# Performance work log

Measured on AMD Instinct MI355X. Metric: run time of the kernel, lower is better.

Reference implementation:

```python
import jax, jax.numpy as jnp
import numpy as np

B, T, HID, NH = 8, 4096, 768, 12
HD = HID // NH          # 64
WIN = 128 // 2          # half window = 64 (local_attention=128)
BLK = 64                # block size == half window
THETA = 10000.0         # local_rope_theta
ATTN_SCALING = 1.0      # default rope type


def setup_inputs() -> dict:
    key = jax.random.key(0)
    k1, k2, k3 = jax.random.split(key, 3)
    hidden_states = jax.random.normal(k1, (B, T, HID), jnp.float32)
    attention_mask = jnp.ones((B, T), jnp.bool_)
    Wqkv = jax.random.normal(k2, (3 * HID, HID), jnp.float32) * 0.02
    Wo = jax.random.normal(k3, (HID, HID), jnp.float32) * 0.02
    return {"hidden_states": hidden_states, "attention_mask": attention_mask,
            "Wqkv": Wqkv, "Wo": Wo}


def _rope(x):
    # x: [B, T, NH, HD]; interleaved-pair complex rotation (pairs = reshape(HD//2, 2))
    pos = jnp.arange(T, dtype=jnp.float32)
    inv_freq = 1.0 / (THETA ** (jnp.arange(0, HD, 2, dtype=jnp.float32) / HD))  # [HD/2]
    ang = pos[:, None] * inv_freq[None, :]                 # [T, HD/2]
    cos = jnp.cos(ang)[None, :, None, :]
    sin = jnp.sin(ang)[None, :, None, :]
    pairs = x.reshape(x.shape[:-1] + (HD // 2, 2))
    a, b = pairs[..., 0], pairs[..., 1]
    ra = a * cos - b * sin
    rb = a * sin + b * cos
    return (jnp.stack([ra, rb], axis=-1).reshape(x.shape)) * ATTN_SCALING


def reference(hidden_states, attention_mask, Wqkv, Wo):
    # fused QKV projection (no bias: attention_bias=False)
    qkv = hidden_states @ Wqkv.T                            # [B, T, 3*HID]
    qkv = qkv.reshape(B, T, 3, NH, HD)
    q, k, v = qkv[:, :, 0], qkv[:, :, 1], qkv[:, :, 2]      # [B, T, NH, HD]
    q = _rope(q)
    k = _rope(k)

    # Blocked sliding-window attention: block = 64, each query block attends
    # key blocks {i-1, i, i+1}; exact +/-64 band enforced by mask.
    nb = T // BLK
    pad = [(0, 0), (BLK, BLK), (0, 0), (0, 0)]
    kp = jnp.pad(k, pad)
    vp = jnp.pad(v, pad)
    kb = kp.reshape(B, nb + 2, BLK, NH, HD)
    vb = vp.reshape(B, nb + 2, BLK, NH, HD)
    knb = jnp.concatenate([kb[:, :-2], kb[:, 1:-1], kb[:, 2:]], axis=2)  # [B, nb, 3*BLK, NH, HD]
    vnb = jnp.concatenate([vb[:, :-2], vb[:, 1:-1], vb[:, 2:]], axis=2)
    qb = q.reshape(B, nb, BLK, NH, HD)

    scores = jnp.einsum('bnqhd,bnkhd->bhnqk', qb, knb) / jnp.sqrt(jnp.float32(HD))
    band = jnp.abs(BLK + jnp.arange(BLK)[:, None] - jnp.arange(3 * BLK)[None, :]) <= WIN  # [BLK, 3*BLK]
    mp = jnp.pad(attention_mask.astype(jnp.bool_), [(0, 0), (BLK, BLK)])
    mb = mp.reshape(B, nb + 2, BLK)
    mnb = jnp.concatenate([mb[:, :-2], mb[:, 1:-1], mb[:, 2:]], axis=2)  # [B, nb, 3*BLK]
    mask = band[None, None, None] & mnb[:, None, :, None, :]
    scores = jnp.where(mask, scores, -jnp.inf)
    probs = jax.nn.softmax(scores, axis=-1)
    out = jnp.einsum('bhnqk,bnkhd->bnqhd', probs, vnb)      # [B, nb, BLK, NH, HD]
    out = out.reshape(B, T, HID)
    return out @ Wo.T
```

## Files before the change

kernel.cpp:

```cpp
#include <hip/hip_runtime.h>
#include <hip/hip_bf16.h>

#define T_SEQ 4096
#define NH 12

typedef __bf16 bf16x8 __attribute__((ext_vector_type(8)));
typedef float f32x4 __attribute__((ext_vector_type(4)));
typedef unsigned int uint32;

__device__ __forceinline__ void gload_lds16(const void* g, void* lds) {
    __builtin_amdgcn_global_load_lds((const __attribute__((address_space(1))) void*)g,
                                     (__attribute__((address_space(3))) void*)lds,
                                     16, 0, 0);
}

__device__ __forceinline__ f32x4 mfma16(bf16x8 a, bf16x8 b, f32x4 c) {
    return __builtin_amdgcn_mfma_f32_16x16x32_bf16(a, b, c, 0, 0, 0);
}

__device__ __forceinline__ void store_out(__hip_bfloat16* p, float v) { *p = __float2bfloat16(v); }
__device__ __forceinline__ void store_out(float* p, float v) { *p = v; }

__global__ __launch_bounds__(256) void f32_to_bf16_kernel(const float* __restrict__ src,
                                                          __hip_bfloat16* __restrict__ dst,
                                                          long n8) {
    long i = (long)blockIdx.x * 256 + threadIdx.x;
    if (i >= n8) return;
    float4 a = *(const float4*)(src + i * 8);
    float4 b = *(const float4*)(src + i * 8 + 4);
    __hip_bfloat16 o[8];
    o[0] = __float2bfloat16(a.x); o[1] = __float2bfloat16(a.y);
    o[2] = __float2bfloat16(a.z); o[3] = __float2bfloat16(a.w);
    o[4] = __float2bfloat16(b.x); o[5] = __float2bfloat16(b.y);
    o[6] = __float2bfloat16(b.z); o[7] = __float2bfloat16(b.w);
    *(uint4*)(dst + i * 8) = *(uint4*)o;
}

__global__ __launch_bounds__(256) void prep_kernel(const float* __restrict__ Wqkv,
                                                   const float* __restrict__ Wo,
                                                   __hip_bfloat16* __restrict__ wqkv_bf,
                                                   __hip_bfloat16* __restrict__ wo_bf,
                                                   float2* __restrict__ tab) {
    long i = (long)blockIdx.x * 256 + threadIdx.x;
    if (i < 221184) {
        const float* s = Wqkv + i * 8;
        __hip_bfloat16* d = wqkv_bf + i * 8;
        float4 a = *(const float4*)s, b = *(const float4*)(s + 4);
        __hip_bfloat16 o[8];
        o[0]=__float2bfloat16(a.x); o[1]=__float2bfloat16(a.y);
        o[2]=__float2bfloat16(a.z); o[3]=__float2bfloat16(a.w);
        o[4]=__float2bfloat16(b.x); o[5]=__float2bfloat16(b.y);
        o[6]=__float2bfloat16(b.z); o[7]=__float2bfloat16(b.w);
        *(uint4*)d = *(uint4*)o;
    } else if (i < 294912) {
        long j = i - 221184;
        const float* s = Wo + j * 8;
        __hip_bfloat16* d = wo_bf + j * 8;
        float4 a = *(const float4*)s, b = *(const float4*)(s + 4);
        __hip_bfloat16 o[8];
        o[0]=__float2bfloat16(a.x); o[1]=__float2bfloat16(a.y);
        o[2]=__float2bfloat16(a.z); o[3]=__float2bfloat16(a.w);
        o[4]=__float2bfloat16(b.x); o[5]=__float2bfloat16(b.y);
        o[6]=__float2bfloat16(b.z); o[7]=__float2bfloat16(b.w);
        *(uint4*)d = *(uint4*)o;
    } else if (i < 425984) {
        long j = i - 294912;
        int tpos = (int)(j >> 5), k = (int)(j & 31);
        float invf = powf(10000.0f, -(2.0f * k) / 64.0f);
        float ang = (float)tpos * invf;
        tab[j] = make_float2((float)cos((double)ang), (float)sin((double)ang));
    }
}

template <typename OutT, int K>
__global__ __launch_bounds__(256) void gemm_nt(const __hip_bfloat16* __restrict__ A,
                                               const __hip_bfloat16* __restrict__ Bw,
                                               OutT* __restrict__ C,
                                               int M, int N, int nbn) {
    __shared__ __align__(16) __hip_bfloat16 As[128 * 64];
    __shared__ __align__(16) __hip_bfloat16 Bs[128 * 64];
    const int tid = threadIdx.x;
    const int w = tid >> 6, l = tid & 63;
    const int g = l >> 4, li = l & 15;
    const int wr = w >> 1, wc = w & 1;

    const int cpx = gridDim.x >> 3;
    const int bid = blockIdx.x;
    const int swz = (bid & 7) * cpx + (bid >> 3);
    const int bm = swz / nbn, bn = swz % nbn;

    const long abase = (long)bm * 128 * K;
    const long bbase = (long)bn * 128 * K;

    f32x4 acc[4][4] = {};

#pragma unroll
    for (int k0 = 0; k0 < K; k0 += 64) {
#pragma unroll
        for (int i = 0; i < 4; ++i) {
            int seg = i * 256 + tid;
            int row = seg >> 3;
            int chunk = seg & 7;
            int schunk = chunk ^ (row & 7);
            int segb = i * 256 + (tid & ~63);
            gload_lds16(A + abase + (long)row * K + k0 + schunk * 8, (char*)As + (size_t)segb * 16);
            gload_lds16(Bw + bbase + (long)row * K + k0 + schunk * 8, (char*)Bs + (size_t)segb * 16);
        }
        __syncthreads();
#pragma unroll
        for (int kk = 0; kk < 64; kk += 32) {
            bf16x8 af[4], bfr[4];
#pragma unroll
            for (int mi = 0; mi < 4; ++mi) {
                const int row = wr * 64 + mi * 16 + li;
                const int gc = (kk >> 3) + g;
                af[mi] = *(const bf16x8*)((char*)As + row * 128 + ((gc ^ (row & 7)) << 4));
            }
#pragma unroll
            for (int ni = 0; ni < 4; ++ni) {
                const int row = wc * 64 + ni * 16 + li;
                const int gc = (kk >> 3) + g;
                bfr[ni] = *(const bf16x8*)((char*)Bs + row * 128 + ((gc ^ (row & 7)) << 4));
            }
#pragma unroll
            for (int mi = 0; mi < 4; ++mi)
#pragma unroll
                for (int ni = 0; ni < 4; ++ni)
                    acc[mi][ni] = mfma16(af[mi], bfr[ni], acc[mi][ni]);
        }
        __syncthreads();
    }

#pragma unroll
    for (int mi = 0; mi < 4; ++mi)
#pragma unroll
        for (int ni = 0; ni < 4; ++ni)
#pragma unroll
            for (int r = 0; r < 4; ++r) {
                long row = (long)bm * 128 + wr * 64 + mi * 16 + g * 4 + r;
                int col = bn * 128 + wc * 64 + ni * 16 + li;
                store_out(&C[row * (long)N + col], acc[mi][ni][r]);
            }
}

__global__ __launch_bounds__(256) void attn_kernel(const __hip_bfloat16* __restrict__ qkv,
                                                   __hip_bfloat16* __restrict__ attn_out,
                                                   const float2* __restrict__ tab) {
    __shared__ __align__(16) __hip_bfloat16 Ks[192 * 72];
    __shared__ __align__(16) __hip_bfloat16 Vs[64 * 200];
    __hip_bfloat16* Ps = Ks;

    const int tid = threadIdx.x;
    const int w = tid >> 6, l = tid & 63;
    const int g = l >> 4, li = l & 15;
    const int mw = w * 16;
    const int ni0 = w & ~1;

    const int cpx = gridDim.x >> 3;
    const int pbid = blockIdx.x;
    const int bid = (pbid & 7) * cpx + (pbid >> 3);

    const int n = bid & 63;
    const int bh = bid >> 6;
    const int b = bh / NH, h = bh % NH;

    const long tokq0 = (long)b * T_SEQ + n * 64;
    const long rowbase = (long)b * T_SEQ;

    const int qrow_t = n * 64 + mw + li;
    uint4 qraw[2];
    float2 qcs[2][4];
#pragma unroll
    for (int ss = 0; ss < 2; ++ss) {
        qraw[ss] = *(const uint4*)&qkv[(rowbase + qrow_t) * 2304 + h * 64 + ss * 32 + g * 8];
#pragma unroll
        for (int j = 0; j < 4; ++j)
            qcs[ss][j] = tab[qrow_t * 32 + ss * 16 + g * 4 + j];
    }

#pragma unroll
    for (int i = 0; i < 6; ++i) {
        int seg = i * 256 + tid;
        int row = seg >> 3, c = (seg & 7) * 8;
        int tk = n * 64 - 64 + row;
        tk = tk < 0 ? 0 : (tk > T_SEQ - 1 ? T_SEQ - 1 : tk);
        uint4 v = *(const uint4*)&qkv[(rowbase + tk) * 2304 + 768 + h * 64 + c];
        __hip_bfloat16 tmp[8], outv[8];
        *(uint4*)tmp = v;
#pragma unroll
        for (int j = 0; j < 4; ++j) {
            float2 cs = tab[tk * 32 + (c >> 1) + j];
            float a = __bfloat162float(tmp[2 * j]), bb = __bfloat162float(tmp[2 * j + 1]);
            outv[2 * j]     = __float2bfloat16(a * cs.x - bb * cs.y);
            outv[2 * j + 1] = __float2bfloat16(a * cs.y + bb * cs.x);
        }
        *(uint4*)&Ks[row * 72 + c] = *(uint4*)outv;
    }
    uint4 vreg[6];
#pragma unroll
    for (int i = 0; i < 6; ++i) {
        int seg = i * 256 + tid;
        int row = seg >> 3, c = (seg & 7) * 8;
        int tk = n * 64 - 64 + row;
        tk = tk < 0 ? 0 : (tk > T_SEQ - 1 ? T_SEQ - 1 : tk);
        vreg[i] = *(const uint4*)&qkv[(rowbase + tk) * 2304 + 1536 + h * 64 + c];
    }

    bf16x8 aq[2];
#pragma unroll
    for (int ss = 0; ss < 2; ++ss) {
        __hip_bfloat16 tmp[8], outv[8];
        *(uint4*)tmp = qraw[ss];
#pragma unroll
        for (int j = 0; j < 4; ++j) {
            float2 cs = qcs[ss][j];
            float a = __bfloat162float(tmp[2 * j]), bb = __bfloat162float(tmp[2 * j + 1]);
            outv[2 * j]     = __float2bfloat16(a * cs.x - bb * cs.y);
            outv[2 * j + 1] = __float2bfloat16(a * cs.y + bb * cs.x);
        }
        aq[ss] = *(bf16x8*)outv;
    }

    __syncthreads();

    f32x4 s[10] = {};
#pragma unroll
    for (int ss = 0; ss < 2; ++ss) {
#pragma unroll
        for (int t = 0; t < 10; ++t) {
            bf16x8 bk = *(const bf16x8*)&Ks[((ni0 + t) * 16 + li) * 72 + ss * 32 + g * 8];
            s[t] = mfma16(aq[ss], bk, s[t]);
        }
    }

#pragma unroll
    for (int i = 0; i < 6; ++i) {
        int seg = i * 256 + tid;
        int row = seg >> 3, c = (seg & 7) * 8;
        __hip_bfloat16 tmp[8];
        *(uint4*)tmp = vreg[i];
#pragma unroll
        for (int j = 0; j < 8; ++j) Vs[(c + j) * 200 + row] = tmp[j];
    }

#pragma unroll
    for (int r = 0; r < 4; ++r) {
        int q = mw + g * 4 + r;
        float mx = -1e30f;
#pragma unroll
        for (int t = 0; t < 10; ++t) {
            int k = (ni0 + t) * 16 + li;
            int kpos = n * 64 - 64 + k;
            bool valid = (k >= q) && (k <= q + 128) && (kpos >= 0) && (kpos < T_SEQ);
            float v = valid ? s[t][r] * 0.125f : -1e30f;
            s[t][r] = v;
            mx = fmaxf(mx, v);
        }
#pragma unroll
        for (int m = 1; m < 16; m <<= 1) mx = fmaxf(mx, __shfl_xor(mx, m, 64));
        float sum = 0.f;
#pragma unroll
        for (int t = 0; t < 10; ++t) {
            float e = __expf(s[t][r] - mx);
            s[t][r] = e;
            sum += e;
        }
#pragma unroll
        for (int m = 1; m < 16; m <<= 1) sum += __shfl_xor(sum, m, 64);
        float inv = 1.0f / sum;
#pragma unroll
        for (int t = 0; t < 10; ++t) s[t][r] *= inv;
    }
    __syncthreads();

#pragma unroll
    for (int r = 0; r < 4; ++r) {
        int q = mw + g * 4 + r;
#pragma unroll
        for (int t = 0; t < 10; ++t)
            Ps[q * 200 + (ni0 + t) * 16 + li] = __float2bfloat16(s[t][r]);
    }
    __syncthreads();

    f32x4 o[4] = {};
#pragma unroll
    for (int c5 = 0; c5 < 5; ++c5) {
        const int kk = ni0 * 16 + c5 * 32;
        bf16x8 ap = *(const bf16x8*)&Ps[(mw + li) * 200 + kk + g * 8];
#pragma unroll
        for (int ni = 0; ni < 4; ++ni) {
            bf16x8 bv = *(const bf16x8*)&Vs[(ni * 16 + li) * 200 + kk + g * 8];
            o[ni] = mfma16(ap, bv, o[ni]);
        }
    }
#pragma unroll
    for (int ni = 0; ni < 4; ++ni)
#pragma unroll
        for (int r = 0; r < 4; ++r) {
            int q = mw + g * 4 + r;
            attn_out[(tokq0 + q) * 768 + h * 64 + ni * 16 + li] = __float2bfloat16(o[ni][r]);
        }
}

extern "C" void kernel_launch(void* const* d_in, const int* in_sizes, int n_in,
                              void* d_out, int out_size, void* d_ws, size_t ws_size,
                              hipStream_t stream) {
    const float* hidden = (const float*)d_in[0];
    const float* Wqkv = (const float*)d_in[2];
    const float* Wo   = (const float*)d_in[3];
    float* out = (float*)d_out;

    char* ws = (char*)d_ws;
    __hip_bfloat16* qkv     = (__hip_bfloat16*)ws;
    __hip_bfloat16* abuf    = (__hip_bfloat16*)(ws + 150994944L);
    __hip_bfloat16* wqkv_bf = (__hip_bfloat16*)(ws + 201326592L);
    __hip_bfloat16* wo_bf   = (__hip_bfloat16*)(ws + 204865536L);
    float2*         tab     = (float2*)(ws + 206045184L);

    f32_to_bf16_kernel<<<12288, 256, 0, stream>>>(hidden, abuf, 3145728);
    prep_kernel<<<1664, 256, 0, stream>>>(Wqkv, Wo, wqkv_bf, wo_bf, tab);

    gemm_nt<__hip_bfloat16, 768><<<4608, 256, 0, stream>>>(abuf, wqkv_bf, qkv, 32768, 2304, 18);
    attn_kernel<<<6144, 256, 0, stream>>>(qkv, abuf, tab);
    gemm_nt<float, 768><<<1536, 256, 0, stream>>>(abuf, wo_bf, out, 32768, 768, 6);
}
```

Measured before the change: 317.6 us.

## Keep softmax probabilities in registers via transposed MFMA and permuted V layout

```diff
diff --git a/kernel.cpp b/kernel.cpp
--- a/kernel.cpp
+++ b/kernel.cpp
@@ -148,13 +148,11 @@
                                                    const float2* __restrict__ tab) {
     __shared__ __align__(16) __hip_bfloat16 Ks[192 * 72];
     __shared__ __align__(16) __hip_bfloat16 Vs[64 * 200];
-    __hip_bfloat16* Ps = Ks;
 
     const int tid = threadIdx.x;
     const int w = tid >> 6, l = tid & 63;
     const int g = l >> 4, li = l & 15;
     const int mw = w * 16;
-    const int ni0 = w & ~1;
 
     const int cpx = gridDim.x >> 3;
     const int pbid = blockIdx.x;
@@ -215,21 +213,21 @@
         for (int j = 0; j < 4; ++j) {
             float2 cs = qcs[ss][j];
             float a = __bfloat162float(tmp[2 * j]), bb = __bfloat162float(tmp[2 * j + 1]);
-            outv[2 * j]     = __float2bfloat16(a * cs.x - bb * cs.y);
-            outv[2 * j + 1] = __float2bfloat16(a * cs.y + bb * cs.x);
+            outv[2 * j]     = __float2bfloat16((a * cs.x - bb * cs.y) * 0.125f);
+            outv[2 * j + 1] = __float2bfloat16((a * cs.y + bb * cs.x) * 0.125f);
         }
         aq[ss] = *(bf16x8*)outv;
     }
 
     __syncthreads();
 
-    f32x4 s[10] = {};
+    f32x4 s[12] = {};
 #pragma unroll
     for (int ss = 0; ss < 2; ++ss) {
 #pragma unroll
-        for (int t = 0; t < 10; ++t) {
-            bf16x8 bk = *(const bf16x8*)&Ks[((ni0 + t) * 16 + li) * 72 + ss * 32 + g * 8];
-            s[t] = mfma16(aq[ss], bk, s[t]);
+        for (int t = 0; t < 12; ++t) {
+            bf16x8 bk = *(const bf16x8*)&Ks[(t * 16 + li) * 72 + ss * 32 + g * 8];
+            s[t] = mfma16(bk, aq[ss], s[t]);
         }
     }
 
@@ -237,69 +235,70 @@
     for (int i = 0; i < 6; ++i) {
         int seg = i * 256 + tid;
         int row = seg >> 3, c = (seg & 7) * 8;
+        int slot = (row & ~31) | (((row >> 2) & 3) << 3) | (((row >> 4) & 1) << 2) | (row & 3);
         __hip_bfloat16 tmp[8];
         *(uint4*)tmp = vreg[i];
 #pragma unroll
-        for (int j = 0; j < 8; ++j) Vs[(c + j) * 200 + row] = tmp[j];
-    }
-
-#pragma unroll
-    for (int r = 0; r < 4; ++r) {
-        int q = mw + g * 4 + r;
-        float mx = -1e30f;
-#pragma unroll
-        for (int t = 0; t < 10; ++t) {
-            int k = (ni0 + t) * 16 + li;
+        for (int j = 0; j < 8; ++j) Vs[(c + j) * 200 + slot] = tmp[j];
+    }
+
+    const int qloc = mw + li;
+    float mx = -1e30f;
+#pragma unroll
+    for (int t = 0; t < 12; ++t)
+#pragma unroll
+        for (int r = 0; r < 4; ++r) {
+            int k = t * 16 + g * 4 + r;
             int kpos = n * 64 - 64 + k;
-            bool valid = (k >= q) && (k <= q + 128) && (kpos >= 0) && (kpos < T_SEQ);
-            float v = valid ? s[t][r] * 0.125f : -1e30f;
+            bool valid = (k >= qloc) && (k <= qloc + 128) && (kpos >= 0) && (kpos < T_SEQ);
+            float v = valid ? s[t][r] : -1e30f;
             s[t][r] = v;
             mx = fmaxf(mx, v);
         }
-#pragma unroll
-        for (int m = 1; m < 16; m <<= 1) mx = fmaxf(mx, __shfl_xor(mx, m, 64));
-        float sum = 0.f;
-#pragma unroll
-        for (int t = 0; t < 10; ++t) {
+    mx = fmaxf(mx, __shfl_xor(mx, 16, 64));
+    mx = fmaxf(mx, __shfl_xor(mx, 32, 64));
+    float sum = 0.f;
+#pragma unroll
+    for (int t = 0; t < 12; ++t)
+#pragma unroll
+        for (int r = 0; r < 4; ++r) {
             float e = __expf(s[t][r] - mx);
             s[t][r] = e;
             sum += e;
         }
-#pragma unroll
-        for (int m = 1; m < 16; m <<= 1) sum += __shfl_xor(sum, m, 64);
-        float inv = 1.0f / sum;
-#pragma unroll
-        for (int t = 0; t < 10; ++t) s[t][r] *= inv;
-    }
+    sum += __shfl_xor(sum, 16, 64);
+    sum += __shfl_xor(sum, 32, 64);
+    const float inv = 1.0f / sum;
+
+    bf16x8 pa[6];
+#pragma unroll
+    for (int c = 0; c < 6; ++c) {
+        __hip_bfloat16 t8[8];
+#pragma unroll
+        for (int m = 0; m < 4; ++m) {
+            t8[m]     = __float2bfloat16(s[2 * c][m] * inv);
+            t8[4 + m] = __float2bfloat16(s[2 * c + 1][m] * inv);
+        }
+        pa[c] = *(bf16x8*)t8;
+    }
+
     __syncthreads();
 
-#pragma unroll
-    for (int r = 0; r < 4; ++r) {
-        int q = mw + g * 4 + r;
-#pragma unroll
-        for (int t = 0; t < 10; ++t)
-            Ps[q * 200 + (ni0 + t) * 16 + li] = __float2bfloat16(s[t][r]);
-    }
-    __syncthreads();
-
     f32x4 o[4] = {};
 #pragma unroll
-    for (int c5 = 0; c5 < 5; ++c5) {
-        const int kk = ni0 * 16 + c5 * 32;
-        bf16x8 ap = *(const bf16x8*)&Ps[(mw + li) * 200 + kk + g * 8];
+    for (int c = 0; c < 6; ++c)
 #pragma unroll
         for (int ni = 0; ni < 4; ++ni) {
-            bf16x8 bv = *(const bf16x8*)&Vs[(ni * 16 + li) * 200 + kk + g * 8];
-            o[ni] = mfma16(ap, bv, o[ni]);
-        }
-    }
-#pragma unroll
-    for (int ni = 0; ni < 4; ++ni)
-#pragma unroll
-        for (int r = 0; r < 4; ++r) {
-            int q = mw + g * 4 + r;
-            attn_out[(tokq0 + q) * 768 + h * 64 + ni * 16 + li] = __float2bfloat16(o[ni][r]);
-        }
+            bf16x8 av = *(const bf16x8*)&Vs[(ni * 16 + li) * 200 + c * 32 + g * 8];
+            o[ni] = mfma16(av, pa[c], o[ni]);
+        }
+#pragma unroll
+    for (int ni = 0; ni < 4; ++ni) {
+        __hip_bfloat16 ov[4];
+#pragma unroll
+        for (int r = 0; r < 4; ++r) ov[r] = __float2bfloat16(o[ni][r]);
+        *(uint2*)&attn_out[(tokq0 + mw + li) * 768 + h * 64 + ni * 16 + g * 4] = *(uint2*)ov;
+    }
 }
 
 extern "C" void kernel_launch(void* const* d_in, const int* in_sizes, int n_in,
```

Result: faster. 288.3 us (-9.2%).
